# Optimization experiments

Measured on AMD Instinct MI355X. Metric: run time of the kernel, lower is better.

The kernel has to match this reference:

```python
import jax, jax.numpy as jnp
import numpy as np

B, CIN, COUT, H, W, K, S, P = 16, 256, 128, 64, 64, 4, 2, 1
PAD = K - 1 - P  # transposed-conv equivalent padding for the lhs-dilated conv


def setup_inputs() -> dict:
    key = jax.random.key(0)
    ks = jax.random.split(key, 13)
    return {
        "x": jax.random.normal(ks[0], (B, CIN, H, W), jnp.float32),
        "feature": jax.random.uniform(ks[1], (B, 4), jnp.float32),
        "weight": jax.random.normal(ks[2], (CIN, COUT, K, K), jnp.float32) * 0.05,
        "t_bayer": jax.random.normal(ks[3], (1, CIN, COUT, K, K), jnp.float32) * 0.05,
        "t_quad": jax.random.normal(ks[4], (1, CIN, COUT, K, K), jnp.float32) * 0.05,
        "t_nano": jax.random.normal(ks[5], (1, CIN, COUT, K, K), jnp.float32) * 0.05,
        "t_qxq": jax.random.normal(ks[6], (1, CIN, COUT, K, K), jnp.float32) * 0.05,
        "m_bayer": jax.random.uniform(ks[7], (1, CIN, COUT, 1, 1), jnp.float32),
        "m_quad": jax.random.uniform(ks[8], (1, CIN, COUT, 1, 1), jnp.float32),
        "m_nano": jax.random.uniform(ks[9], (1, CIN, COUT, 1, 1), jnp.float32),
        "m_qxq": jax.random.uniform(ks[10], (1, CIN, COUT, 1, 1), jnp.float32),
        "bias": jax.random.normal(ks[11], (COUT,), jnp.float32) * 0.05,
        "prelu_a": jnp.full((1,), 0.25, jnp.float32),
    }


def _synth_weights(feature, weight, t_bayer, t_quad, t_nano, t_qxq,
                   m_bayer, m_quad, m_nano, m_qxq):
    # feature: (B,4) softmax attention -> (B,4,1,1,1)
    sa = feature[:, :, None, None, None]
    dyn = (t_bayer * m_bayer * sa[:, 0:1]
           + t_quad * m_quad * sa[:, 1:2]
           + t_nano * m_nano * sa[:, 2:3]
           + t_qxq * m_qxq * sa[:, 3:4])  # (B, CIN, COUT, K, K)
    return weight[None] + dyn  # broadcast base weight over batch


def _deconv_per_sample(xi, wi):
    # xi: (CIN,H,W); wi: (CIN,COUT,K,K) torch conv_transpose layout.
    # conv_transpose == lhs-dilated conv with spatially-flipped, transposed kernel
    kern = jnp.flip(jnp.swapaxes(wi, 0, 1), axis=(-2, -1))  # (COUT,CIN,K,K)
    out = jax.lax.conv_general_dilated(
        xi[None], kern, window_strides=(1, 1),
        padding=[(PAD, PAD), (PAD, PAD)], lhs_dilation=(S, S),
        dimension_numbers=("NCHW", "OIHW", "NCHW"))
    return out[0]  # (COUT, H*S, W*S)


def reference(x, feature, weight, t_bayer, t_quad, t_nano, t_qxq,
              m_bayer, m_quad, m_nano, m_qxq, bias, prelu_a):
    w = _synth_weights(feature, weight, t_bayer, t_quad, t_nano, t_qxq,
                       m_bayer, m_quad, m_nano, m_qxq)
    out = jax.vmap(_deconv_per_sample)(x, w)  # (B, COUT, 128, 128)
    out = out + bias[None, :, None, None]
    # PReLU with single shared slope (torch default init 0.25)
    return jnp.where(out >= 0, out, prelu_a[0] * out)
```

## Files before the change

### kernel.cpp

```cpp
#include <hip/hip_runtime.h>
#include <hip/hip_bf16.h>
#include <cstddef>
#include <cstdint>

#define B_    16
#define CIN_  256
#define COUT_ 128
#define H_    64
#define W_    64
#define OH_   128
#define OW_   128

#define AST   44
#define ACHUNK (128*AST)
#define ABYTES (ACHUNK*2)

typedef __attribute__((ext_vector_type(8))) short bf16x8;
typedef __attribute__((ext_vector_type(4))) float f32x4;

__device__ inline short f2bf(float f) {
    __hip_bfloat16 h = __float2bfloat16(f);
    return *reinterpret_cast<short*>(&h);
}

__device__ inline void async_ld16(const void* g, void* l) {
    typedef const __attribute__((address_space(1))) unsigned int* gp_t;
    typedef __attribute__((address_space(3))) unsigned int* lp_t;
    __builtin_amdgcn_global_load_lds((gp_t)g, (lp_t)l, 16, 0, 0);
}

__device__ inline void synth_body(
    int chunk, int cog, int b, int tid,
    const float* __restrict__ weight,
    const float* __restrict__ tb, const float* __restrict__ tq,
    const float* __restrict__ tn, const float* __restrict__ tx,
    const float* __restrict__ mb, const float* __restrict__ mq,
    const float* __restrict__ mn, const float* __restrict__ mx,
    const float* __restrict__ feat,
    short* __restrict__ aws,
    short* lbuf )
{
    const int ci0 = chunk * 8;
    const float f0 = feat[b*4+0], f1 = feat[b*4+1];
    const float f2 = feat[b*4+2], f3 = feat[b*4+3];

    #pragma unroll
    for (int it = 0; it < 4; ++it) {
        int e4   = tid + it*256;
        int ci_l = e4 >> 7;
        int rem  = e4 & 127;
        int co_l = rem >> 2;
        int kh   = rem & 3;
        int co   = cog*32 + co_l;
        int base = (ci0 + ci_l) * COUT_ + co;
        float4 w4 = *(const float4*)(weight + (size_t)base*16 + kh*4);
        float4 b4 = *(const float4*)(tb + (size_t)base*16 + kh*4);
        float4 q4 = *(const float4*)(tq + (size_t)base*16 + kh*4);
        float4 n4 = *(const float4*)(tn + (size_t)base*16 + kh*4);
        float4 x4 = *(const float4*)(tx + (size_t)base*16 + kh*4);
        const float* wp = (const float*)&w4;
        const float* bp = (const float*)&b4;
        const float* qp = (const float*)&q4;
        const float* np = (const float*)&n4;
        const float* xp = (const float*)&x4;
        float sb = mb[base]*f0, sq = mq[base]*f1;
        float sn = mn[base]*f2, sx = mx[base]*f3;
        int r  = (kh+1)&1;
        int dh = (kh<2) ? 1 : 0;
        #pragma unroll
        for (int kw = 0; kw < 4; ++kw) {
            int s  = (kw+1)&1;
            int dw = (kw<2) ? 1 : 0;
            float v = wp[kw] + sb*bp[kw] + sq*qp[kw] + sn*np[kw] + sx*xp[kw];
            lbuf[((r*2+s)*32 + co_l)*AST + (dh*2+dw)*8 + ci_l] = f2bf(v);
        }
    }
    __syncthreads();
    for (int j = tid; j < 4*176; j += 256) {
        int cls = j / 176; int jj = j - cls*176;
        size_t dst = (((size_t)(b*4 + cls)*32 + chunk)*128 + cog*32) * AST;
        *(int4*)(aws + dst + (size_t)jj*8) =
            *(const int4*)(lbuf + cls*32*AST + jj*8);
    }
}

__device__ inline void transform_body(
    int ihp, int b, int tid,
    const float* __restrict__ x, short* __restrict__ xt,
    float* xls )
{
    const int4 z4 = {0, 0, 0, 0};

    if (ihp == 0 || ihp == 65) {
        for (int j = tid; j < 2112; j += 256) {
            int c = j / 66, iwp = j - c*66;
            *(int4*)(xt + ((((size_t)b*32 + c)*66 + ihp)*66 + iwp)*8) = z4;
        }
        return;
    }
    if (tid < 64) {
        int c = tid >> 1, iwp = (tid & 1) * 65;
        *(int4*)(xt + ((((size_t)b*32 + c)*66 + ihp)*66 + iwp)*8) = z4;
    }
    const int ih = ihp - 1;
    for (int half = 0; half < 2; ++half) {
        __syncthreads();
        #pragma unroll
        for (int it = 0; it < 8; ++it) {
            int ci_l = it*16 + (tid >> 4);
            int iw4  = (tid & 15) * 4;
            float4 v = *(const float4*)(
                x + (((size_t)b*256 + half*128 + ci_l)*64 + ih)*64 + iw4);
            *(float4*)(xls + ci_l*68 + iw4) = v;
        }
        __syncthreads();
        #pragma unroll
        for (int it2 = 0; it2 < 4; ++it2) {
            int chunk_l = it2*4 + (tid >> 6);
            int chunk   = half*16 + chunk_l;
            int iw      = tid & 63;
            short s8[8];
            #pragma unroll
            for (int j = 0; j < 8; ++j)
                s8[j] = f2bf(xls[(chunk_l*8 + j)*68 + iw]);
            *(int4*)(xt + ((((size_t)b*32 + chunk)*66 + ihp)*66 + (iw+1))*8)
                = *(const int4*)s8;
        }
    }
}

__global__ __launch_bounds__(256) void prep_fused(
    const float* __restrict__ x,
    const float* __restrict__ weight,
    const float* __restrict__ tb, const float* __restrict__ tq,
    const float* __restrict__ tn, const float* __restrict__ tx,
    const float* __restrict__ mb, const float* __restrict__ mq,
    const float* __restrict__ mn, const float* __restrict__ mx,
    const float* __restrict__ feat,
    short* __restrict__ aws, short* __restrict__ xt)
{
    __shared__ __align__(16) char smem[34816];
    const int bid = blockIdx.x;
    const int tid = threadIdx.x;
    if (bid < 1056) {
        int ihp = bid % 66, b = bid / 66;
        transform_body(ihp, b, tid, x, xt, (float*)smem);
    } else {
        int sb = bid - 1056;
        int chunk = sb & 31, cog = (sb >> 5) & 3, b = sb >> 7;
        synth_body(chunk, cog, b, tid, weight, tb, tq, tn, tx,
                   mb, mq, mn, mx, feat, aws, (short*)smem);
    }
}

__global__ __launch_bounds__(256) void synth_aws(
    const float* __restrict__ weight,
    const float* __restrict__ tb, const float* __restrict__ tq,
    const float* __restrict__ tn, const float* __restrict__ tx,
    const float* __restrict__ mb, const float* __restrict__ mq,
    const float* __restrict__ mn, const float* __restrict__ mx,
    const float* __restrict__ feat,
    short* __restrict__ aws)
{
    __shared__ __align__(16) short lbuf[4][32][AST];
    const int chunk = blockIdx.x, cog = blockIdx.y, b = blockIdx.z;
    synth_body(chunk, cog, b, threadIdx.x, weight, tb, tq, tn, tx,
               mb, mq, mn, mx, feat, aws, &lbuf[0][0][0]);
}

__global__ __launch_bounds__(256) void deconv_mfma2(
    const short* __restrict__ aws, const short* __restrict__ xt,
    const float* __restrict__ bias, const float* __restrict__ prelu_a,
    float* __restrict__ out)
{
    const int tid  = threadIdx.x;
    const int lane = tid & 63;
    const int wv   = tid >> 6;
    const int wm   = wv & 1, wn = wv >> 1;
    const int o    = blockIdx.x;
    const int n    = (o & 7) * 256 + (o >> 3);
    const int nt   = n & 31;
    const int cls  = (n >> 5) & 3;
    const int b    = n >> 7;
    const int a0 = (nt >> 2) * 8, c0 = (nt & 3) * 16;
    const int r = cls >> 1, s = cls & 1;

    __shared__ __align__(16) short als[2][ACHUNK];
    __shared__ __align__(16) short xsb[2][1536];

    const short* gb[4]; int gstep[4], loff[4], isB[4], act[4];
    {
        const size_t awb = (((size_t)b*4 + cls)*32) * ACHUNK;
        #pragma unroll
        for (int i = 0; i < 4; ++i) {
            int t = wv + i*4;
            act[i] = (t < 14);
            if (t < 11) {
                gb[i]    = aws + awb + t*512 + lane*8;
                gstep[i] = ACHUNK;  loff[i] = t*512;  isB[i] = 0;
            } else {
                int j = t - 11;
                int p = j*64 + lane; if (p > 152) p = 152;
                int row = p / 17, col = p - row*17;
                gb[i] = xt + (((size_t)b*32*66 + (a0 + r + row))*66
                              + (c0 + s + col)) * 8;
                gstep[i] = 66*66*8;  loff[i] = j*512;  isB[i] = 1;
            }
        }
    }

    f32x4 acc[4][4];
    #pragma unroll
    for (int mi = 0; mi < 4; ++mi)
        #pragma unroll
        for (int ni = 0; ni < 4; ++ni)
            acc[mi][ni] = (f32x4){0.f, 0.f, 0.f, 0.f};

    const int nlo = lane & 15;
    const int q   = lane >> 4;
    const int dh  = q >> 1, dw = q & 1;

    #pragma unroll
    for (int i = 0; i < 4; ++i)
        if (act[i])
            async_ld16(gb[i], isB[i] ? &xsb[0][loff[i]] : &als[0][loff[i]]);

    for (int c = 0; c < 32; ++c) {
        __syncthreads();
        const int sel = c & 1;
        if (c < 31) {
            const int ps = sel ^ 1;
            #pragma unroll
            for (int i = 0; i < 4; ++i)
                if (act[i])
                    async_ld16(gb[i] + (size_t)(c+1)*gstep[i],
                               isB[i] ? &xsb[ps][loff[i]] : &als[ps][loff[i]]);
        }
        bf16x8 af[4], bfr[4];
        #pragma unroll
        for (int mi = 0; mi < 4; ++mi)
            af[mi] = *(const bf16x8*)(&als[sel][(wm*64 + mi*16 + nlo)*AST + q*8]);
        #pragma unroll
        for (int ni = 0; ni < 4; ++ni) {
            int a_local = wn*4 + ni;
            bfr[ni] = *(const bf16x8*)(&xsb[sel][((a_local + dh)*17 + (nlo + dw))*8]);
        }
        #pragma unroll
        for (int mi = 0; mi < 4; ++mi)
            #pragma unroll
            for (int ni = 0; ni < 4; ++ni)
                acc[mi][ni] = __builtin_amdgcn_mfma_f32_16x16x32_bf16(
                    af[mi], bfr[ni], acc[mi][ni], 0, 0, 0);
    }

    const float pa = prelu_a[0];
    #pragma unroll
    for (int mi = 0; mi < 4; ++mi) {
        #pragma unroll
        for (int reg = 0; reg < 4; ++reg) {
            int co = wm*64 + mi*16 + q*4 + reg;
            float bv = bias[co];
            #pragma unroll
            for (int ni = 0; ni < 4; ++ni) {
                int a_local = wn*4 + ni;
                int oh = 2*(a0 + a_local) + r;
                int ow = 2*(c0 + nlo) + s;
                float v = acc[mi][ni][reg] + bv;
                v = (v >= 0.f) ? v : pa*v;
                out[(((size_t)b*COUT_ + co)*OH_ + oh)*OW_ + ow] = v;
            }
        }
    }
}

__global__ __launch_bounds__(256, 2) void deconv_mfma_gather(
    const float* __restrict__ x,
    const short* __restrict__ aws,
    const float* __restrict__ bias,
    const float* __restrict__ prelu_a,
    float* __restrict__ out)
{
    const int tid  = threadIdx.x;
    const int lane = tid & 63;
    const int wv   = tid >> 6;
    const int wm   = wv & 1, wn = wv >> 1;
    const int nt   = blockIdx.x;
    const int cls  = blockIdx.y;
    const int b    = blockIdx.z;
    const int a0 = (nt >> 2) * 8, c0 = (nt & 3) * 16;
    const int r = cls >> 1, s = cls & 1;

    __shared__ __align__(16) short xs[1280];
    __shared__ __align__(16) short als[ACHUNK];

    int goff[5], gstep[5], gok[5];
    #pragma unroll
    for (int i = 0; i < 5; ++i) {
        int e    = tid + i*256;
        int ci_l = e & 7;
        int rc   = e >> 3;
        int row  = rc / 17;
        int col  = rc - row*17;
        int ih   = a0 - 1 + r + row;
        int iw   = c0 - 1 + s + col;
        int ok   = (rc < 153) && ((unsigned)ih < (unsigned)H_)
                              && ((unsigned)iw < (unsigned)W_);
        goff[i]  = ok ? (((b*CIN_ + ci_l)*H_ + ih)*W_ + iw) : 0;
        gstep[i] = ok ? (8*H_*W_) : 0;
        gok[i]   = ok;
    }
    const size_t aws_base = (((size_t)b*4 + cls)*32) * ACHUNK;

    f32x4 acc[4][4];
    #pragma unroll
    for (int mi = 0; mi < 4; ++mi)
        #pragma unroll
        for (int ni = 0; ni < 4; ++ni)
            acc[mi][ni] = (f32x4){0.f, 0.f, 0.f, 0.f};

    const int nlo = lane & 15;
    const int q   = lane >> 4;
    const int dh  = q >> 1, dw = q & 1;

    for (int chunk = 0; chunk < 32; ++chunk) {
        __syncthreads();
        #pragma unroll
        for (int i = 0; i < 5; ++i) {
            float v = x[goff[i] + chunk*gstep[i]];
            v = gok[i] ? v : 0.0f;
            xs[tid + i*256] = f2bf(v);
        }
        {
            const short* src = aws + aws_base + (size_t)chunk*ACHUNK;
            #pragma unroll
            for (int i = 0; i < 3; ++i) {
                int idx = wv + i*4;
                if (idx < 11)
                    async_ld16(src + idx*512 + lane*8, als + idx*512);
            }
        }
        __syncthreads();
        bf16x8 af[4], bfr[4];
        #pragma unroll
        for (int mi = 0; mi < 4; ++mi)
            af[mi] = *(const bf16x8*)(als + (wm*64 + mi*16 + nlo)*AST + q*8);
        #pragma unroll
        for (int ni = 0; ni < 4; ++ni) {
            int a_local = wn*4 + ni;
            bfr[ni] = *(const bf16x8*)(xs + ((a_local + dh)*17 + (nlo + dw))*8);
        }
        #pragma unroll
        for (int mi = 0; mi < 4; ++mi)
            #pragma unroll
            for (int ni = 0; ni < 4; ++ni)
                acc[mi][ni] = __builtin_amdgcn_mfma_f32_16x16x32_bf16(
                    af[mi], bfr[ni], acc[mi][ni], 0, 0, 0);
    }

    const float pa = prelu_a[0];
    #pragma unroll
    for (int mi = 0; mi < 4; ++mi) {
        #pragma unroll
        for (int reg = 0; reg < 4; ++reg) {
            int co = wm*64 + mi*16 + q*4 + reg;
            float bv = bias[co];
            #pragma unroll
            for (int ni = 0; ni < 4; ++ni) {
                int a_local = wn*4 + ni;
                int oh = 2*(a0 + a_local) + r;
                int ow = 2*(c0 + nlo) + s;
                float v = acc[mi][ni][reg] + bv;
                v = (v >= 0.f) ? v : pa*v;
                out[(((size_t)b*COUT_ + co)*OH_ + oh)*OW_ + ow] = v;
            }
        }
    }
}

__global__ __launch_bounds__(256) void deconv_fallback(
    const float* __restrict__ x,
    const float* __restrict__ weight,
    const float* __restrict__ tb, const float* __restrict__ tq,
    const float* __restrict__ tn, const float* __restrict__ tx,
    const float* __restrict__ mb, const float* __restrict__ mq,
    const float* __restrict__ mn, const float* __restrict__ mx,
    const float* __restrict__ feat,
    const float* __restrict__ bias, const float* __restrict__ prelu_a,
    float* __restrict__ out)
{
    const int tid    = threadIdx.x;
    const int tile   = blockIdx.x;
    const int coT    = blockIdx.y;
    const int b      = blockIdx.z;
    const int tile_h = tile >> 3, tile_w = tile & 7;
    const int a0 = tile_h * 8;
    const int c0 = tile_w * 8;
    const int co0 = coT * 64;

    const int tco = tid & 15;
    const int tpx = tid >> 4;
    const int rr  = tpx >> 2, rc = tpx & 3;

    __shared__ float xsf[4][100];
    __shared__ float wsh[4][16][64];

    float acc[4][4][4];
    #pragma unroll
    for (int i = 0; i < 4; ++i)
        #pragma unroll
        for (int j = 0; j < 4; ++j)
            #pragma unroll
            for (int c = 0; c < 4; ++c) acc[i][j][c] = 0.f;

    float f0 = feat[b*4 + 0], f1 = feat[b*4 + 1];
    float f2 = feat[b*4 + 2], f3 = feat[b*4 + 3];

    for (int chunk = 0; chunk < CIN_ / 4; ++chunk) {
        const int ci0 = chunk * 4;
        __syncthreads();
        for (int e = tid; e < 400; e += 256) {
            int ci_l = e / 100; int rem = e - ci_l * 100;
            int rI = rem / 10;  int cI = rem - rI * 10;
            int ih = a0 - 1 + rI, iw = c0 - 1 + cI;
            float v = 0.f;
            if ((unsigned)ih < (unsigned)H_ && (unsigned)iw < (unsigned)W_)
                v = x[(((size_t)b * CIN_ + ci0 + ci_l) * H_ + ih) * W_ + iw];
            xsf[ci_l][rem] = v;
        }
        #pragma unroll
        for (int k = 0; k < 4; ++k) {
            int g = tid + k * 256;
            int ci_l = g >> 8; int rrem = g & 255;
            int co_l = rrem >> 2; int tg = (rrem & 3) * 4;
            int cico = (ci0 + ci_l) * COUT_ + co0 + co_l;
            int e = cico * 16 + tg;
            float4 w  = *(const float4*)(weight + e);
            float4 vb = *(const float4*)(tb + e);
            float4 vq = *(const float4*)(tq + e);
            float4 vn = *(const float4*)(tn + e);
            float4 vx = *(const float4*)(tx + e);
            float sb = mb[cico] * f0, sq = mq[cico] * f1;
            float sn = mn[cico] * f2, sx = mx[cico] * f3;
            float4 wvv;
            wvv.x = w.x + sb*vb.x + sq*vq.x + sn*vn.x + sx*vx.x;
            wvv.y = w.y + sb*vb.y + sq*vq.y + sn*vn.y + sx*vx.y;
            wvv.z = w.z + sb*vb.z + sq*vq.z + sn*vn.z + sx*vx.z;
            wvv.w = w.w + sb*vb.w + sq*vq.w + sn*vn.w + sx*vx.w;
            wsh[ci_l][tg + 0][co_l] = wvv.x;
            wsh[ci_l][tg + 1][co_l] = wvv.y;
            wsh[ci_l][tg + 2][co_l] = wvv.z;
            wsh[ci_l][tg + 3][co_l] = wvv.w;
        }
        __syncthreads();
        #pragma unroll
        for (int ci_l = 0; ci_l < 4; ++ci_l) {
            float xpv[4][4];
            #pragma unroll
            for (int i = 0; i < 4; ++i)
                #pragma unroll
                for (int j = 0; j < 4; ++j)
                    xpv[i][j] = xsf[ci_l][(rr*2 + i) * 10 + rc*2 + j];
            #pragma unroll
            for (int kh = 0; kh < 4; ++kh) {
                const int rpar = (kh & 1) ? 0 : 1;
                const int offh = (kh == 0) ? 2 : (kh == 3) ? 0 : 1;
                #pragma unroll
                for (int kw = 0; kw < 4; ++kw) {
                    const int spar = (kw & 1) ? 0 : 1;
                    const int offw = (kw == 0) ? 2 : (kw == 3) ? 0 : 1;
                    float4 wvv = *(const float4*)&wsh[ci_l][kh*4 + kw][tco*4];
                    float wr[4] = {wvv.x, wvv.y, wvv.z, wvv.w};
                    #pragma unroll
                    for (int da = 0; da < 2; ++da)
                        #pragma unroll
                        for (int dc = 0; dc < 2; ++dc) {
                            const float xvv = xpv[da + offh][dc + offw];
                            #pragma unroll
                            for (int cc = 0; cc < 4; ++cc)
                                acc[2*da + rpar][2*dc + spar][cc] =
                                    fmaf(wr[cc], xvv, acc[2*da + rpar][2*dc + spar][cc]);
                        }
                }
            }
        }
    }
    const float pa  = prelu_a[0];
    const int oh0 = tile_h * 16 + rr * 4;
    const int ow0 = tile_w * 16 + rc * 4;
    #pragma unroll
    for (int cc = 0; cc < 4; ++cc) {
        const int co = co0 + tco * 4 + cc;
        const float bv = bias[co];
        #pragma unroll
        for (int dr = 0; dr < 4; ++dr)
            #pragma unroll
            for (int dw2 = 0; dw2 < 4; ++dw2) {
                float v = acc[dr][dw2][cc] + bv;
                v = (v >= 0.f) ? v : pa * v;
                out[(((size_t)b * COUT_ + co) * OH_ + (oh0 + dr)) * OW_ + (ow0 + dw2)] = v;
            }
    }
}

extern "C" void kernel_launch(void* const* d_in, const int* in_sizes, int n_in,
                              void* d_out, int out_size, void* d_ws, size_t ws_size,
                              hipStream_t stream) {
    (void)in_sizes; (void)n_in; (void)out_size;
    const float* x      = (const float*)d_in[0];
    const float* feat   = (const float*)d_in[1];
    const float* weight = (const float*)d_in[2];
    const float* tb     = (const float*)d_in[3];
    const float* tq     = (const float*)d_in[4];
    const float* tn     = (const float*)d_in[5];
    const float* tx     = (const float*)d_in[6];
    const float* mb     = (const float*)d_in[7];
    const float* mq     = (const float*)d_in[8];
    const float* mn     = (const float*)d_in[9];
    const float* mx     = (const float*)d_in[10];
    const float* bias   = (const float*)d_in[11];
    const float* prelu  = (const float*)d_in[12];
    float* out = (float*)d_out;

    const size_t aws_sz = (size_t)B_ * 4 * 32 * 128 * AST * sizeof(short);
    const size_t xt_sz  = (size_t)B_ * 32 * 66 * 66 * 8 * sizeof(short);

    if (ws_size >= aws_sz + xt_sz) {
        short* aws = (short*)d_ws;
        short* xt  = (short*)((char*)d_ws + aws_sz);
        prep_fused<<<dim3(1056 + 2048), 256, 0, stream>>>(
            x, weight, tb, tq, tn, tx, mb, mq, mn, mx, feat, aws, xt);
        deconv_mfma2<<<dim3(2048), 256, 0, stream>>>(
            aws, xt, bias, prelu, out);
    } else if (ws_size >= aws_sz) {
        short* aws = (short*)d_ws;
        synth_aws<<<dim3(32, 4, 16), 256, 0, stream>>>(
            weight, tb, tq, tn, tx, mb, mq, mn, mx, feat, aws);
        deconv_mfma_gather<<<dim3(32, 4, 16), 256, 0, stream>>>(
            x, aws, bias, prelu, out);
    } else {
        deconv_fallback<<<dim3(64, 2, 16), 256, 0, stream>>>(
            x, weight, tb, tq, tn, tx, mb, mq, mn, mx, feat, bias, prelu, out);
    }
}
```

Baseline: 321.0 us.

## Reuse loaded template weights across all batches in synth and remap deconv block order

The weight-synthesis body now loads each base/template weight slice once per block and loops over all 16 batch samples, instead of launching a separate block per batch that reloads the same template data. This cuts global reads of the five weight tensors by up to the batch factor and shrinks the prep grid from 2048 to 512 synth blocks, at the cost of a serial batch loop with two barriers per iteration. The deconv kernel's block-to-tile mapping is also changed so each group of eight consecutive blocks covers different batch pairs with class innermost, which alters L2 and cache locality for the weight and input tiles.

Measured after the change: 285.8 us. -11.0%, faster.

```diff
diff --git a/kernel.cpp b/kernel.cpp
--- a/kernel.cpp
+++ b/kernel.cpp
@@ -13,7 +13,6 @@
 
 #define AST   44
 #define ACHUNK (128*AST)
-#define ABYTES (ACHUNK*2)
 
 typedef __attribute__((ext_vector_type(8))) short bf16x8;
 typedef __attribute__((ext_vector_type(4))) float f32x4;
@@ -30,7 +29,7 @@
 }
 
 __device__ inline void synth_body(
-    int chunk, int cog, int b, int tid,
+    int chunk, int cog8, int tid,
     const float* __restrict__ weight,
     const float* __restrict__ tb, const float* __restrict__ tq,
     const float* __restrict__ tn, const float* __restrict__ tx,
@@ -40,47 +39,49 @@
     short* __restrict__ aws,
     short* lbuf )
 {
-    const int ci0 = chunk * 8;
-    const float f0 = feat[b*4+0], f1 = feat[b*4+1];
-    const float f2 = feat[b*4+2], f3 = feat[b*4+3];
-
-    #pragma unroll
-    for (int it = 0; it < 4; ++it) {
-        int e4   = tid + it*256;
-        int ci_l = e4 >> 7;
-        int rem  = e4 & 127;
-        int co_l = rem >> 2;
-        int kh   = rem & 3;
-        int co   = cog*32 + co_l;
-        int base = (ci0 + ci_l) * COUT_ + co;
-        float4 w4 = *(const float4*)(weight + (size_t)base*16 + kh*4);
-        float4 b4 = *(const float4*)(tb + (size_t)base*16 + kh*4);
-        float4 q4 = *(const float4*)(tq + (size_t)base*16 + kh*4);
-        float4 n4 = *(const float4*)(tn + (size_t)base*16 + kh*4);
-        float4 x4 = *(const float4*)(tx + (size_t)base*16 + kh*4);
-        const float* wp = (const float*)&w4;
-        const float* bp = (const float*)&b4;
-        const float* qp = (const float*)&q4;
-        const float* np = (const float*)&n4;
-        const float* xp = (const float*)&x4;
-        float sb = mb[base]*f0, sq = mq[base]*f1;
-        float sn = mn[base]*f2, sx = mx[base]*f3;
-        int r  = (kh+1)&1;
-        int dh = (kh<2) ? 1 : 0;
+    const int ci_l = tid >> 5;
+    const int co_l = (tid >> 2) & 7;
+    const int kh   = tid & 3;
+    const int base = (chunk*8 + ci_l) * COUT_ + cog8*8 + co_l;
+
+    const float4 w4 = *(const float4*)(weight + (size_t)base*16 + kh*4);
+    const float4 b4 = *(const float4*)(tb + (size_t)base*16 + kh*4);
+    const float4 q4 = *(const float4*)(tq + (size_t)base*16 + kh*4);
+    const float4 n4 = *(const float4*)(tn + (size_t)base*16 + kh*4);
+    const float4 x4 = *(const float4*)(tx + (size_t)base*16 + kh*4);
+    const float m_b = mb[base], m_q = mq[base];
+    const float m_n = mn[base], m_x = mx[base];
+    const float* wp = (const float*)&w4;
+    const float* bp = (const float*)&b4;
+    const float* qp = (const float*)&q4;
+    const float* np = (const float*)&n4;
+    const float* xp = (const float*)&x4;
+
+    const int r  = (kh+1)&1;
+    const int dh = (kh<2) ? 1 : 0;
+
+    for (int b = 0; b < 16; ++b) {
+        const float sb = m_b * feat[b*4+0];
+        const float sq = m_q * feat[b*4+1];
+        const float sn = m_n * feat[b*4+2];
+        const float sx = m_x * feat[b*4+3];
         #pragma unroll
         for (int kw = 0; kw < 4; ++kw) {
             int s  = (kw+1)&1;
             int dw = (kw<2) ? 1 : 0;
             float v = wp[kw] + sb*bp[kw] + sq*qp[kw] + sn*np[kw] + sx*xp[kw];
-            lbuf[((r*2+s)*32 + co_l)*AST + (dh*2+dw)*8 + ci_l] = f2bf(v);
-        }
-    }
-    __syncthreads();
-    for (int j = tid; j < 4*176; j += 256) {
-        int cls = j / 176; int jj = j - cls*176;
-        size_t dst = (((size_t)(b*4 + cls)*32 + chunk)*128 + cog*32) * AST;
-        *(int4*)(aws + dst + (size_t)jj*8) =
-            *(const int4*)(lbuf + cls*32*AST + jj*8);
+            lbuf[((r*2+s)*8 + co_l)*32 + (dh*2+dw)*8 + ci_l] = f2bf(v);
+        }
+        __syncthreads();
+        if (tid < 128) {
+            int cls  = tid >> 5;
+            int j    = tid & 31;
+            int co_r = j >> 2, t4 = j & 3;
+            size_t dst = ((((size_t)(b*4 + cls)*32 + chunk)*128)
+                          + cog8*8 + co_r) * AST + t4*8;
+            *(int4*)(aws + dst) = *(const int4*)(lbuf + (cls*8 + co_r)*32 + t4*8);
+        }
+        __syncthreads();
     }
 }
 
@@ -147,8 +148,8 @@
         transform_body(ihp, b, tid, x, xt, (float*)smem);
     } else {
         int sb = bid - 1056;
-        int chunk = sb & 31, cog = (sb >> 5) & 3, b = sb >> 7;
-        synth_body(chunk, cog, b, tid, weight, tb, tq, tn, tx,
+        int chunk = sb & 31, cog8 = sb >> 5;
+        synth_body(chunk, cog8, tid, weight, tb, tq, tn, tx,
                    mb, mq, mn, mx, feat, aws, (short*)smem);
     }
 }
@@ -162,9 +163,8 @@
     const float* __restrict__ feat,
     short* __restrict__ aws)
 {
-    __shared__ __align__(16) short lbuf[4][32][AST];
-    const int chunk = blockIdx.x, cog = blockIdx.y, b = blockIdx.z;
-    synth_body(chunk, cog, b, threadIdx.x, weight, tb, tq, tn, tx,
+    __shared__ __align__(16) short lbuf[4][8][32];
+    synth_body(blockIdx.x, blockIdx.y, threadIdx.x, weight, tb, tq, tn, tx,
                mb, mq, mn, mx, feat, aws, &lbuf[0][0][0]);
 }
 
@@ -178,10 +178,11 @@
     const int wv   = tid >> 6;
     const int wm   = wv & 1, wn = wv >> 1;
     const int o    = blockIdx.x;
-    const int n    = (o & 7) * 256 + (o >> 3);
-    const int nt   = n & 31;
-    const int cls  = (n >> 5) & 3;
-    const int b    = n >> 7;
+    const int x8   = o & 7;
+    const int l    = o >> 3;
+    const int cls  = l & 3;
+    const int nt   = (l >> 2) & 31;
+    const int b    = 2*x8 + (l >> 7);
     const int a0 = (nt >> 2) * 8, c0 = (nt & 3) * 16;
     const int r = cls >> 1, s = cls & 1;
 
@@ -527,13 +528,13 @@
     if (ws_size >= aws_sz + xt_sz) {
         short* aws = (short*)d_ws;
         short* xt  = (short*)((char*)d_ws + aws_sz);
-        prep_fused<<<dim3(1056 + 2048), 256, 0, stream>>>(
+        prep_fused<<<dim3(1056 + 512), 256, 0, stream>>>(
             x, weight, tb, tq, tn, tx, mb, mq, mn, mx, feat, aws, xt);
         deconv_mfma2<<<dim3(2048), 256, 0, stream>>>(
             aws, xt, bias, prelu, out);
     } else if (ws_size >= aws_sz) {
         short* aws = (short*)d_ws;
-        synth_aws<<<dim3(32, 4, 16), 256, 0, stream>>>(
+        synth_aws<<<dim3(32, 16), 256, 0, stream>>>(
             weight, tb, tq, tn, tx, mb, mq, mn, mx, feat, aws);
         deconv_mfma_gather<<<dim3(32, 4, 16), 256, 0, stream>>>(
             x, aws, bias, prelu, out);
```
